# Kernel tuning notes

Hardware: AMD Instinct MI355X
Metric: run time of the kernel (lower is better)

The kernel has to match this reference:

```python
import jax, jax.numpy as jnp
import numpy as np

PERIOD = 0.1


def setup_inputs() -> dict:
    key = jax.random.key(0)
    ks = jax.random.split(key, 16)
    B, N, C, P = 2, 3072, 4, 4
    E, H, T, F, L = 512, 8, 256, 64, 4
    Nt = N // P

    def rn(k, shape, scale=0.02):
        return jax.random.normal(k, shape, jnp.float32) * scale

    return {
        "x": jax.random.normal(ks[0], (B, N, C), jnp.float32),
        "t": jax.random.normal(ks[1], (B, T), jnp.float32),
        "vec_map": jax.random.normal(ks[2], (B, N, 3), jnp.float32),
        # RelativeBias dense: freq features -> heads
        "W_rb": rn(ks[3], (F, H)),
        "b_rb": jnp.zeros((H,), jnp.float32),
        # patch embedding dense: P*C -> E
        "W_embed": rn(ks[4], (P * C, E), 0.1),
        "b_embed": jnp.zeros((E,), jnp.float32),
        "pos_emb": rn(ks[5], (Nt, E)),
        # stacked per-block params (leading dim L = n_blocks)
        "ada1_W1": rn(ks[6], (L, T, T)),
        "ada1_b1": jnp.zeros((L, T), jnp.float32),
        "ada1_W2": rn(ks[7], (L, T, 3 * E)),
        "ada1_b2": jnp.zeros((L, 3 * E), jnp.float32),
        "qkv_W": rn(ks[8], (L, E, 3 * E)),
        "qkv_b": jnp.zeros((L, 3 * E), jnp.float32),
        "out_W": rn(ks[9], (L, E, E)),
        "out_b": jnp.zeros((L, E), jnp.float32),
        "ada2_W1": rn(ks[10], (L, T, T)),
        "ada2_b1": jnp.zeros((L, T), jnp.float32),
        "ada2_W2": rn(ks[11], (L, T, 3 * E)),
        "ada2_b2": jnp.zeros((L, 3 * E), jnp.float32),
        "mlp_W1": rn(ks[12], (L, E, 4 * E)),
        "mlp_b1": jnp.zeros((L, 4 * E), jnp.float32),
        "mlp_W2": rn(ks[13], (L, 4 * E, E)),
        "mlp_b2": jnp.zeros((L, E), jnp.float32),
    }


def _layernorm(y):
    # flax LayerNorm(use_bias=False, use_scale=False), eps=1e-6
    mu = jnp.mean(y, axis=-1, keepdims=True)
    var = jnp.mean(jnp.square(y - mu), axis=-1, keepdims=True)
    return (y - mu) * jax.lax.rsqrt(var + 1e-6)


def _adaln(t, W1, b1, W2, b2):
    h = jax.nn.silu(t @ W1 + b1)
    m = (h @ W2 + b2)[..., None, :]  # (B, 1, 3E)
    return jnp.split(m, 3, axis=-1)


def reference(x, t, vec_map, W_rb, b_rb, W_embed, b_embed, pos_emb,
              ada1_W1, ada1_b1, ada1_W2, ada1_b2, qkv_W, qkv_b, out_W, out_b,
              ada2_W1, ada2_b1, ada2_W2, ada2_b2, mlp_W1, mlp_b1, mlp_W2, mlp_b2):
    B, N, C = x.shape
    Nt, E = pos_emb.shape
    P = N // Nt
    F, H = W_rb.shape
    hd = E // H

    # patchify tokens: (B, N, C) -> (B, Nt, P*C); mean vec per patch
    xp = x.reshape(B, Nt, P * C)
    vp = vec_map.reshape(B, Nt, P, 3).mean(axis=-2)

    # relative bias logits (B, Nt, Nt, H)
    v = vp / jnp.linalg.norm(vp, axis=-1, keepdims=True)
    dif = v[..., :, None, :] - v[..., None, :, :]
    dot = 1.0 - 0.5 * jnp.sum(dif * dif, axis=-1)
    angle = jnp.arccos(jnp.clip(dot, -1.0, 1.0)) / 0.005
    freqs = jnp.linspace(0, 1, F // 2) / PERIOD
    ph = freqs * angle[..., None]  # (B, Nt, Nt, F/2)
    pos = jnp.concatenate((jnp.sin(ph), jnp.cos(ph)), axis=-1)
    bias = pos @ W_rb + b_rb

    # patch embed + learned positional embedding
    h0 = xp @ W_embed + b_embed + pos_emb
    inv_sqrt_hd = 1.0 / jnp.sqrt(jnp.float32(hd))

    def block(xc, params):
        (aW1, ab1, aW2, ab2, qW, qb, oW, ob,
         cW1, cb1, cW2, cb2, mW1, mb1, mW2, mb2) = params
        g1, be1, al1 = _adaln(t, aW1, ab1, aW2, ab2)
        y = (g1 + 1.0) * _layernorm(xc) + be1
        qkv = (y @ qW + qb).reshape(B, Nt, H, 3, hd)
        q, k, vv = qkv[..., 0, :], qkv[..., 1, :], qkv[..., 2, :]
        logits = jnp.einsum('bqht,bkht->bqkh', q, k) * inv_sqrt_hd + bias
        logits = logits - jnp.max(logits, axis=-2, keepdims=True)
        attn = jax.nn.softmax(logits, axis=-2)  # softmax over keys (K axis)
        y = jnp.einsum('bqkh,bkht->bqht', attn, vv).reshape(B, Nt, E)
        y = y @ oW + ob
        xc = xc + al1 * y / jnp.sqrt(1.0 + al1 * al1)
        g2, be2, al2 = _adaln(t, cW1, cb1, cW2, cb2)
        y = (g2 + 1.0) * _layernorm(xc) + be2
        y = jax.nn.gelu(y @ mW1 + mb1) @ mW2 + mb2
        xc = xc + al2 * y / jnp.sqrt(1.0 + al2 * al2)
        return xc, None

    params = (ada1_W1, ada1_b1, ada1_W2, ada1_b2, qkv_W, qkv_b, out_W, out_b,
              ada2_W1, ada2_b1, ada2_W2, ada2_b2, mlp_W1, mlp_b1, mlp_W2, mlp_b2)
    out, _ = jax.lax.scan(block, h0, params)
    return out
```

## Files before the change

kernel.cpp:

```cpp
#include <hip/hip_runtime.h>
#include <hip/hip_bf16.h>


#define NT 768
#define EDIM 512
#define E3 1536
#define E4 2048
#define NH 8
#define TB 2

typedef unsigned short ushort_t;
typedef __attribute__((ext_vector_type(8))) short bf16x8;
typedef __attribute__((ext_vector_type(4))) float f32x4;

__device__ inline float b2f(ushort_t u) {
    unsigned int i = ((unsigned int)u) << 16; float f;
    __builtin_memcpy(&f, &i, 4); return f;
}
__device__ inline ushort_t f2b(float f) {
    __hip_bfloat16 h = __float2bfloat16(f);
    ushort_t u; __builtin_memcpy(&u, &h, 2); return u;
}
__device__ inline float gelu_tanh(float u) {
    float z = 1.5957691216057308f * (u + 0.044715f * u * u * u);
    z = fminf(z, 40.f);
    float t = __expf(z);
    float th = (t - 1.f) / (t + 1.f);
    return 0.5f * u * (1.f + th);
}

__global__ __launch_bounds__(256) void k_vnorm(const float* __restrict__ vm, float* __restrict__ v) {
    int idx = blockIdx.x * 256 + threadIdx.x;
    if (idx >= TB * NT) return;
    float s0 = 0.f, s1 = 0.f, s2 = 0.f;
    #pragma unroll
    for (int p = 0; p < 4; ++p) {
        s0 += vm[(idx * 4 + p) * 3 + 0];
        s1 += vm[(idx * 4 + p) * 3 + 1];
        s2 += vm[(idx * 4 + p) * 3 + 2];
    }
    float inv = 1.f / sqrtf(s0 * s0 + s1 * s1 + s2 * s2);
    v[idx * 3 + 0] = s0 * inv; v[idx * 3 + 1] = s1 * inv; v[idx * 3 + 2] = s2 * inv;
}

__global__ __launch_bounds__(256) void k_bias(const float* __restrict__ v, const float* __restrict__ W_rb,
                                              const float* __restrict__ b_rb, ushort_t* __restrict__ biasT) {
    int bq = blockIdx.x; int b = bq / NT, q = bq % NT;
    __shared__ float sv[NT * 3];
    int tid = threadIdx.x, lane = tid & 63, wave = tid >> 6;
    for (int i = tid; i < NT * 3; i += 256) sv[i] = v[b * NT * 3 + i];

    int g = lane >> 4, col = lane & 15;
    ushort_t tw[16];
    #pragma unroll
    for (int j = 0; j < 8; ++j) {
        float wsv = (col < 8) ? W_rb[(g * 8 + j) * 8 + col] : 0.f;
        float wcv = (col < 8) ? W_rb[(32 + g * 8 + j) * 8 + col] : 0.f;
        tw[j] = f2b(wsv); tw[8 + j] = f2b(wcv);
    }
    bf16x8 bsf, bcf;
    __builtin_memcpy(&bsf, tw, 16);
    __builtin_memcpy(&bcf, tw + 8, 16);
    float brh = (col < 8) ? b_rb[col] : 0.f;
    __syncthreads();

    float vq0 = sv[q * 3], vq1 = sv[q * 3 + 1], vq2 = sv[q * 3 + 2];
    float gf = (float)(8 * g);

    for (int it = 0; it < 12; ++it) {
        int tile = (it * 4 + wave) * 16;
        int p = tile + col;
        float d0 = vq0 - sv[p * 3], d1 = vq1 - sv[p * 3 + 1], d2 = vq2 - sv[p * 3 + 2];
        float dot = 1.f - 0.5f * (d0 * d0 + d1 * d1 + d2 * d2);
        dot = fminf(1.f, fmaxf(-1.f, dot));
        float theta = acosf(dot) * (2000.f / 31.f);
        float s1, c1; __sincosf(theta, &s1, &c1);
        float sg, cg; __sincosf(theta * gf, &sg, &cg);
        ushort_t fs[16];
        #pragma unroll
        for (int j = 0; j < 8; ++j) {
            fs[j] = f2b(sg); fs[8 + j] = f2b(cg);
            float ns = sg * c1 + cg * s1;
            cg = cg * c1 - sg * s1;
            sg = ns;
        }
        bf16x8 asf, acf;
        __builtin_memcpy(&asf, fs, 16);
        __builtin_memcpy(&acf, fs + 8, 16);
        f32x4 acc = {0.f, 0.f, 0.f, 0.f};
        acc = __builtin_amdgcn_mfma_f32_16x16x32_bf16(asf, bsf, acc, 0, 0, 0);
        acc = __builtin_amdgcn_mfma_f32_16x16x32_bf16(acf, bcf, acc, 0, 0, 0);
        if (col < 8) {
            ushort_t o[4];
            #pragma unroll
            for (int r = 0; r < 4; ++r) o[r] = f2b(acc[r] + brh);
            long off = (long)(b * 8 + col) * NT * NT + (long)q * NT + tile + 4 * g;
            uint2 pk;
            pk.x = (unsigned int)o[0] | ((unsigned int)o[1] << 16);
            pk.y = (unsigned int)o[2] | ((unsigned int)o[3] << 16);
            *(uint2*)(biasT + off) = pk;
        }
    }
}

__global__ __launch_bounds__(256) void k_embed(const float* __restrict__ x, const float* __restrict__ W,
                                               const float* __restrict__ be, const float* __restrict__ pe,
                                               float* __restrict__ xc) {
    int row = blockIdx.x; int nt = row % NT;
    __shared__ float sx[16];
    int tid = threadIdx.x;
    if (tid < 16) sx[tid] = x[row * 16 + tid];
    __syncthreads();
    for (int e = tid; e < EDIM; e += 256) {
        float a = be[e] + pe[nt * EDIM + e];
        #pragma unroll
        for (int j = 0; j < 16; ++j) a += sx[j] * W[j * EDIM + e];
        xc[(long)row * EDIM + e] = a;
    }
}

__global__ __launch_bounds__(256) void k_adaln(const float* __restrict__ t,
    const float* __restrict__ a1W1, const float* __restrict__ a1b1, const float* __restrict__ a1W2, const float* __restrict__ a1b2,
    const float* __restrict__ a2W1, const float* __restrict__ a2b1, const float* __restrict__ a2W2, const float* __restrict__ a2b2,
    float* __restrict__ ada) {
    int blk = blockIdx.x; int b = blk & 1, lw = blk >> 1; int which = lw & 1, l = lw >> 1;
    const float* W1 = (which ? a2W1 : a1W1) + (long)l * 256 * 256;
    const float* b1 = (which ? a2b1 : a1b1) + l * 256;
    const float* W2 = (which ? a2W2 : a1W2) + (long)l * 256 * E3;
    const float* b2 = (which ? a2b2 : a1b2) + l * E3;
    __shared__ float st[256], sh[256];
    int tid = threadIdx.x;
    st[tid] = t[b * 256 + tid];
    __syncthreads();
    float a = b1[tid];
    for (int i = 0; i < 256; ++i) a += st[i] * W1[i * 256 + tid];
    sh[tid] = a / (1.f + __expf(-a));
    __syncthreads();
    int c = blockIdx.y * 256 + tid;
    float m = b2[c];
    for (int i = 0; i < 256; ++i) m += sh[i] * W2[i * E3 + c];
    ada[(long)(lw * 2 + b) * E3 + c] = m;
}

__global__ __launch_bounds__(256) void k_lnmod(const float* __restrict__ xc, const float* __restrict__ ada,
                                               ushort_t* __restrict__ out, int lw) {
    int row = blockIdx.x; int b = row / NT;
    const float* ap = ada + (long)(lw * 2 + b) * E3;
    int tid = threadIdx.x;
    float2 vv = *(const float2*)(xc + (long)row * EDIM + tid * 2);
    float s1 = vv.x + vv.y, s2 = vv.x * vv.x + vv.y * vv.y;
    for (int o = 32; o; o >>= 1) { s1 += __shfl_down(s1, o); s2 += __shfl_down(s2, o); }
    __shared__ float sr[8];
    if ((tid & 63) == 0) { sr[tid >> 6] = s1; sr[4 + (tid >> 6)] = s2; }
    __syncthreads();
    s1 = sr[0] + sr[1] + sr[2] + sr[3];
    s2 = sr[4] + sr[5] + sr[6] + sr[7];
    float mu = s1 * (1.f / 512.f);
    float var = s2 * (1.f / 512.f) - mu * mu;
    float inv = rsqrtf(var + 1e-6f);
    int e = tid * 2;
    float r0 = (ap[e] + 1.f) * ((vv.x - mu) * inv) + ap[512 + e];
    float r1 = (ap[e + 1] + 1.f) * ((vv.y - mu) * inv) + ap[512 + e + 1];
    unsigned int pk = (unsigned int)f2b(r0) | ((unsigned int)f2b(r1) << 16);
    ((unsigned int*)out)[(long)row * 256 + tid] = pk;
}

__global__ __launch_bounds__(256) void k_softmax(float* __restrict__ logits) {
    float* p = logits + (long)blockIdx.x * NT;
    ushort_t* pb = (ushort_t*)p;
    int tid = threadIdx.x;
    float v0 = p[tid], v1 = p[tid + 256], v2 = p[tid + 512];
    float mx = fmaxf(v0, fmaxf(v1, v2));
    for (int o = 32; o; o >>= 1) mx = fmaxf(mx, __shfl_down(mx, o));
    __shared__ float sr[8];
    if ((tid & 63) == 0) sr[tid >> 6] = mx;
    __syncthreads();
    mx = fmaxf(fmaxf(sr[0], sr[1]), fmaxf(sr[2], sr[3]));
    float e0 = __expf(v0 - mx), e1 = __expf(v1 - mx), e2 = __expf(v2 - mx);
    float s = e0 + e1 + e2;
    for (int o = 32; o; o >>= 1) s += __shfl_down(s, o);
    if ((tid & 63) == 0) sr[4 + (tid >> 6)] = s;
    __syncthreads();
    s = sr[4] + sr[5] + sr[6] + sr[7];
    float inv = 1.f / s;
    pb[tid] = f2b(e0 * inv); pb[tid + 256] = f2b(e1 * inv); pb[tid + 512] = f2b(e2 * inv);
}

__global__ __launch_bounds__(256) void k_wT(const float* __restrict__ W, ushort_t* __restrict__ Wt,
                                            int Kd, int Nd) {
    const float* Wp = W + (long)blockIdx.z * Kd * Nd;
    ushort_t* Wtp = Wt + (long)blockIdx.z * Kd * Nd;
    int n0 = blockIdx.x * 64, k0 = blockIdx.y * 64;
    __shared__ float s[64][65];
    int tid = threadIdx.x;
    #pragma unroll
    for (int it = 0; it < 4; ++it) {
        int idx = tid + it * 256;
        int r = idx >> 4, c4 = (idx & 15) * 4;
        float4 vv = *(const float4*)(Wp + (long)(k0 + r) * Nd + n0 + c4);
        s[r][c4] = vv.x; s[r][c4 + 1] = vv.y; s[r][c4 + 2] = vv.z; s[r][c4 + 3] = vv.w;
    }
    __syncthreads();
    #pragma unroll
    for (int it = 0; it < 4; ++it) {
        int idx = tid + it * 256;
        int rn = idx >> 4, ck = (idx & 15) * 4;
        long base = (long)(n0 + rn) * Kd + k0 + ck;
        #pragma unroll
        for (int j = 0; j < 4; ++j) Wtp[base + j] = f2b(s[ck + j][rn]);
    }
}

__global__ __launch_bounds__(256) void k_vT(const ushort_t* __restrict__ qkv16, ushort_t* __restrict__ vT) {
    int bh = blockIdx.y; int b = bh >> 3, h = bh & 7;
    int nt0 = blockIdx.x * 64;
    __shared__ ushort_t s[64][80];
    int tid = threadIdx.x;
    #pragma unroll
    for (int it = 0; it < 2; ++it) {
        int idx = tid + it * 256;
        int rnt = idx >> 3, c8 = (idx & 7) * 8;
        bf16x8 vv = *(const bf16x8*)(qkv16 + ((long)(b * NT + nt0 + rnt) * E3 + h * 192 + 128 + c8));
        *(bf16x8*)&s[rnt][c8] = vv;
    }
    __syncthreads();
    #pragma unroll
    for (int it = 0; it < 2; ++it) {
        int idx = tid + it * 256;
        int d = idx >> 3, n8 = (idx & 7) * 8;
        ushort_t tmp[8];
        #pragma unroll
        for (int j = 0; j < 8; ++j) tmp[j] = s[n8 + j][d];
        bf16x8 ov; __builtin_memcpy(&ov, tmp, 16);
        *(bf16x8*)(vT + ((long)bh * 64 + d) * NT + nt0 + n8) = ov;
    }
}

__device__ inline void stC(float* C, long i, float v) { C[i] = v; }
__device__ inline void stC(ushort_t* C, long i, float v) { C[i] = f2b(v); }

template<int EPI, typename CT>
__global__ __launch_bounds__(256) void k_mm64(
        const ushort_t* __restrict__ A0, const ushort_t* __restrict__ B0,
        const void* __restrict__ biasbase, CT* __restrict__ C0,
        int Kchunk, int kSplit, int lda, int ldb, int ldc, int ldbias,
        long aB, long aH, long bB, long bH, long cB, long cH, long biB, long biH, long kcStride) {
    int z = blockIdx.z;
    int batch = z / kSplit, kc = z - batch * kSplit;
    int zb = batch >> 3, zh = batch & 7;
    const ushort_t* A = A0 + zb * aB + zh * aH + (long)kc * Kchunk;
    const ushort_t* B = B0 + zb * bB + zh * bH + (long)kc * Kchunk;
    CT* C = C0 + zb * cB + zh * cH + (EPI == 4 ? kc * kcStride : 0);

    __shared__ __align__(16) ushort_t As[64 * 64];
    __shared__ __align__(16) ushort_t Bs[64 * 64];

    int tid = threadIdx.x, lane = tid & 63, wave = tid >> 6;
    int wm = wave >> 1, wn = wave & 1;
    int m0 = blockIdx.y * 64, n0 = blockIdx.x * 64;
    int srow = lane >> 3;
    int scol = ((lane & 7) ^ srow) * 8;

    f32x4 acc[2][2];
    #pragma unroll
    for (int i = 0; i < 2; ++i)
        #pragma unroll
        for (int j = 0; j < 2; ++j) acc[i][j] = f32x4{0.f, 0.f, 0.f, 0.f};

    int r = lane & 15, g = lane >> 4, rs = r & 7;

    for (int k0 = 0; k0 < Kchunk; k0 += 64) {
        #pragma unroll
        for (int c0 = 0; c0 < 4; ++c0) {
            int c = wave * 4 + c0;
            const ushort_t* src;
            ushort_t* dst;
            if (c < 8) {
                src = A + (long)(m0 + c * 8 + srow) * lda + k0 + scol;
                dst = As + c * 512;
            } else {
                src = B + (long)(n0 + (c - 8) * 8 + srow) * ldb + k0 + scol;
                dst = Bs + (c - 8) * 512;
            }
            __builtin_amdgcn_global_load_lds(
                (const __attribute__((address_space(1))) unsigned int*)src,
                (__attribute__((address_space(3))) unsigned int*)dst, 16, 0, 0);
        }
        __syncthreads();
        bf16x8 af[2][2], bfr[2][2];
        #pragma unroll
        for (int i = 0; i < 2; ++i) {
            int row = wm * 32 + i * 16 + r;
            #pragma unroll
            for (int kh = 0; kh < 2; ++kh) {
                int sl = (kh * 4 + g) ^ rs;
                af[i][kh] = *(const bf16x8*)((const char*)As + row * 128 + sl * 16);
            }
        }
        #pragma unroll
        for (int j = 0; j < 2; ++j) {
            int row = wn * 32 + j * 16 + r;
            #pragma unroll
            for (int kh = 0; kh < 2; ++kh) {
                int sl = (kh * 4 + g) ^ rs;
                bfr[j][kh] = *(const bf16x8*)((const char*)Bs + row * 128 + sl * 16);
            }
        }
        #pragma unroll
        for (int kh = 0; kh < 2; ++kh)
            #pragma unroll
            for (int i = 0; i < 2; ++i)
                #pragma unroll
                for (int j = 0; j < 2; ++j)
                    acc[i][j] = __builtin_amdgcn_mfma_f32_16x16x32_bf16(af[i][kh], bfr[j][kh], acc[i][j], 0, 0, 0);
        __syncthreads();
    }

    int gr = (lane >> 4) * 4, cL = lane & 15;
    #pragma unroll
    for (int i = 0; i < 2; ++i) {
        int mB = m0 + wm * 32 + i * 16 + gr;
        #pragma unroll
        for (int j = 0; j < 2; ++j) {
            int n = n0 + wn * 32 + j * 16 + cL;
            float bn = 0.f;
            if constexpr (EPI == 0 || EPI == 1) {
                if (biasbase) bn = ((const float*)biasbase)[n];
            }
            #pragma unroll
            for (int rr = 0; rr < 4; ++rr) {
                float vv = acc[i][j][rr];
                long cidx = (long)(mB + rr) * ldc + n;
                if constexpr (EPI == 0) {
                    stC(C, cidx, vv + bn);
                } else if constexpr (EPI == 1) {
                    stC(C, cidx, gelu_tanh(vv + bn));
                } else if constexpr (EPI == 2) {
                    const ushort_t* bp = (const ushort_t*)biasbase + zb * biB + zh * biH;
                    stC(C, cidx, vv * 0.125f + b2f(bp[(long)(mB + rr) * ldbias + n]));
                } else {
                    stC(C, cidx, vv);
                }
            }
        }
    }
}

__global__ __launch_bounds__(256) void k_red_res(const float* __restrict__ P, int kSplit,
        const float* __restrict__ bias, const float* __restrict__ ada, int lw,
        const float* __restrict__ xin, float* __restrict__ xout) {
    int gidx = blockIdx.x * 256 + threadIdx.x;
    int e4 = gidx * 4;
    int m = e4 >> 9, n = e4 & 511;
    int b = (m >= NT);
    const float* al = ada + (long)(lw * 2 + b) * E3 + 1024;
    float4 s = *(const float4*)(P + e4);
    for (int kc = 1; kc < kSplit; ++kc) {
        float4 p = *(const float4*)(P + (long)kc * 786432 + e4);
        s.x += p.x; s.y += p.y; s.z += p.z; s.w += p.w;
    }
    float4 bv = *(const float4*)(bias + n);
    float4 av = *(const float4*)(al + n);
    float4 xv = *(const float4*)(xin + e4);
    float4 r;
    r.x = xv.x + av.x * rsqrtf(1.f + av.x * av.x) * (s.x + bv.x);
    r.y = xv.y + av.y * rsqrtf(1.f + av.y * av.y) * (s.y + bv.y);
    r.z = xv.z + av.z * rsqrtf(1.f + av.z * av.z) * (s.z + bv.z);
    r.w = xv.w + av.w * rsqrtf(1.f + av.w * av.w) * (s.w + bv.w);
    *(float4*)(xout + e4) = r;
}

__global__ __launch_bounds__(256) void k_red_pv(const float* __restrict__ P, ushort_t* __restrict__ attnb) {
    int blk = blockIdx.x;
    int bh = blk / 48, sub = blk % 48;
    int inner = sub * 256 + threadIdx.x;
    int nt = inner >> 4, d = (inner & 15) * 4;
    long src = (long)bh * 49152 + nt * 64 + d;
    float4 s = *(const float4*)(P + src);
    #pragma unroll
    for (int kc = 1; kc < 4; ++kc) {
        float4 p = *(const float4*)(P + (long)kc * 786432 + src);
        s.x += p.x; s.y += p.y; s.z += p.z; s.w += p.w;
    }
    int b = bh >> 3, h = bh & 7;
    long off = ((long)(b * NT + nt) * EDIM) + h * 64 + d;
    unsigned int p0 = (unsigned int)f2b(s.x) | ((unsigned int)f2b(s.y) << 16);
    unsigned int p1 = (unsigned int)f2b(s.z) | ((unsigned int)f2b(s.w) << 16);
    unsigned int* dst = (unsigned int*)(attnb + off);
    dst[0] = p0; dst[1] = p1;
}

extern "C" void kernel_launch(void* const* d_in, const int* in_sizes, int n_in,
                              void* d_out, int out_size, void* d_ws, size_t ws_size,
                              hipStream_t stream) {
    const float* x       = (const float*)d_in[0];
    const float* t       = (const float*)d_in[1];
    const float* vec_map = (const float*)d_in[2];
    const float* W_rb    = (const float*)d_in[3];
    const float* b_rb    = (const float*)d_in[4];
    const float* W_embed = (const float*)d_in[5];
    const float* b_embed = (const float*)d_in[6];
    const float* pos_emb = (const float*)d_in[7];
    const float* a1W1    = (const float*)d_in[8];
    const float* a1b1    = (const float*)d_in[9];
    const float* a1W2    = (const float*)d_in[10];
    const float* a1b2    = (const float*)d_in[11];
    const float* qkv_W   = (const float*)d_in[12];
    const float* qkv_b   = (const float*)d_in[13];
    const float* out_W   = (const float*)d_in[14];
    const float* out_b   = (const float*)d_in[15];
    const float* a2W1    = (const float*)d_in[16];
    const float* a2b1    = (const float*)d_in[17];
    const float* a2W2    = (const float*)d_in[18];
    const float* a2b2    = (const float*)d_in[19];
    const float* mlp_W1  = (const float*)d_in[20];
    const float* mlp_b1  = (const float*)d_in[21];
    const float* mlp_W2  = (const float*)d_in[22];
    const float* mlp_b2  = (const float*)d_in[23];

    float* ws = (float*)d_ws;
    size_t o = 0;
    float* v        = ws + o; o += 8192;
    ushort_t* biasT = (ushort_t*)(ws + o); o += 4718592;
    float* logits   = ws + o; o += 9437184;
    float* ada      = ws + o; o += 24576;
    float* xc       = ws + o; o += 786432;
    ushort_t* ln16  = (ushort_t*)(ws + o); o += 393216;
    ushort_t* qkv16 = (ushort_t*)(ws + o); o += 1179648;
    ushort_t* vT    = (ushort_t*)(ws + o); o += 393216;
    ushort_t* attnb = (ushort_t*)(ws + o); o += 393216;
    ushort_t* mlph  = (ushort_t*)(ws + o); o += 1572864;
    ushort_t* qkvWt = (ushort_t*)(ws + o); o += 1572864;
    ushort_t* outWt = (ushort_t*)(ws + o); o += 524288;
    ushort_t* mlp1Wt = (ushort_t*)(ws + o); o += 2097152;
    ushort_t* mlp2Wt = (ushort_t*)(ws + o); o += 2097152;
    float* P_pv     = ws + o; o += 3145728;
    float* P_proj   = ws + o; o += 3145728;

    k_vnorm<<<6, 256, 0, stream>>>(vec_map, v);
    k_bias<<<TB * NT, 256, 0, stream>>>(v, W_rb, b_rb, biasT);
    k_embed<<<TB * NT, 256, 0, stream>>>(x, W_embed, b_embed, pos_emb, xc);
    k_adaln<<<dim3(16, 6), 256, 0, stream>>>(t, a1W1, a1b1, a1W2, a1b2, a2W1, a2b1, a2W2, a2b2, ada);
    k_wT<<<dim3(24, 8, 4), 256, 0, stream>>>(qkv_W,  qkvWt,  512, 1536);
    k_wT<<<dim3(8,  8, 4), 256, 0, stream>>>(out_W,  outWt,  512, 512);
    k_wT<<<dim3(32, 8, 4), 256, 0, stream>>>(mlp_W1, mlp1Wt, 512, 2048);
    k_wT<<<dim3(8, 32, 4), 256, 0, stream>>>(mlp_W2, mlp2Wt, 2048, 512);

    const long qB = (long)NT * E3, qH = 192;
    const long lB = (long)NH * NT * NT, lH = (long)NT * NT;
    const long pB = 2 * lB, pH = 2 * lH;
    const long vB = (long)NH * 64 * NT, vH = (long)64 * NT;

    for (int l = 0; l < 4; ++l) {
        int lw0 = l * 2, lw1 = l * 2 + 1;
        k_lnmod<<<TB * NT, 256, 0, stream>>>(xc, ada, ln16, lw0);
        k_mm64<0, ushort_t><<<dim3(24, 24, 1), 256, 0, stream>>>(
            ln16, qkvWt + (long)l * 786432, qkv_b + l * E3, qkv16,
            512, 1, 512, 512, E3, 0, 0, 0, 0, 0, 0, 0, 0, 0, 0);
        k_vT<<<dim3(12, 16), 256, 0, stream>>>(qkv16, vT);
        k_mm64<2, float><<<dim3(12, 12, 16), 256, 0, stream>>>(
            qkv16, qkv16 + 64, biasT, logits,
            64, 1, E3, E3, NT, NT, qB, qH, qB, qH, lB, lH, lB, lH, 0);
        k_softmax<<<TB * NH * NT, 256, 0, stream>>>(logits);
        k_mm64<4, float><<<dim3(1, 12, 64), 256, 0, stream>>>(
            (const ushort_t*)logits, vT, nullptr, P_pv,
            192, 4, E3, NT, 64, 0, pB, pH, vB, vH, (long)NH * 49152, 49152, 0, 0, 786432);
        k_red_pv<<<768, 256, 0, stream>>>(P_pv, attnb);
        k_mm64<4, float><<<dim3(8, 24, 2), 256, 0, stream>>>(
            attnb, outWt + (long)l * 262144, nullptr, P_proj,
            256, 2, 512, 512, EDIM, 0, 0, 0, 0, 0, 0, 0, 0, 0, 786432);
        k_red_res<<<768, 256, 0, stream>>>(P_proj, 2, out_b + l * EDIM, ada, lw0, xc, xc);
        k_lnmod<<<TB * NT, 256, 0, stream>>>(xc, ada, ln16, lw1);
        k_mm64<1, ushort_t><<<dim3(32, 24, 1), 256, 0, stream>>>(
            ln16, mlp1Wt + (long)l * 1048576, mlp_b1 + l * E4, mlph,
            512, 1, 512, 512, E4, 0, 0, 0, 0, 0, 0, 0, 0, 0, 0);
        k_mm64<4, float><<<dim3(8, 24, 4), 256, 0, stream>>>(
            mlph, mlp2Wt + (long)l * 1048576, nullptr, P_proj,
            512, 4, 2048, 2048, EDIM, 0, 0, 0, 0, 0, 0, 0, 0, 0, 786432);
        k_red_res<<<768, 256, 0, stream>>>(P_proj, 4, mlp_b2 + l * EDIM, ada, lw1, xc,
            (l == 3) ? (float*)d_out : xc);
    }
}
```

Measured before the change: 431.1 us.

## Fuse attention into flash-style kernel and switch GEMMs to 128x128 tiles with fused residual epilogue

```diff
diff --git a/kernel.cpp b/kernel.cpp
--- a/kernel.cpp
+++ b/kernel.cpp
@@ -12,6 +12,10 @@
 typedef unsigned short ushort_t;
 typedef __attribute__((ext_vector_type(8))) short bf16x8;
 typedef __attribute__((ext_vector_type(4))) float f32x4;
+
+#define GLOAD(src, dst) __builtin_amdgcn_global_load_lds( \
+    (const __attribute__((address_space(1))) unsigned int*)(src), \
+    (__attribute__((address_space(3))) unsigned int*)(dst), 16, 0, 0)
 
 __device__ inline float b2f(ushort_t u) {
     unsigned int i = ((unsigned int)u) << 16; float f;
@@ -165,27 +169,6 @@
     ((unsigned int*)out)[(long)row * 256 + tid] = pk;
 }
 
-__global__ __launch_bounds__(256) void k_softmax(float* __restrict__ logits) {
-    float* p = logits + (long)blockIdx.x * NT;
-    ushort_t* pb = (ushort_t*)p;
-    int tid = threadIdx.x;
-    float v0 = p[tid], v1 = p[tid + 256], v2 = p[tid + 512];
-    float mx = fmaxf(v0, fmaxf(v1, v2));
-    for (int o = 32; o; o >>= 1) mx = fmaxf(mx, __shfl_down(mx, o));
-    __shared__ float sr[8];
-    if ((tid & 63) == 0) sr[tid >> 6] = mx;
-    __syncthreads();
-    mx = fmaxf(fmaxf(sr[0], sr[1]), fmaxf(sr[2], sr[3]));
-    float e0 = __expf(v0 - mx), e1 = __expf(v1 - mx), e2 = __expf(v2 - mx);
-    float s = e0 + e1 + e2;
-    for (int o = 32; o; o >>= 1) s += __shfl_down(s, o);
-    if ((tid & 63) == 0) sr[4 + (tid >> 6)] = s;
-    __syncthreads();
-    s = sr[4] + sr[5] + sr[6] + sr[7];
-    float inv = 1.f / s;
-    pb[tid] = f2b(e0 * inv); pb[tid + 256] = f2b(e1 * inv); pb[tid + 512] = f2b(e2 * inv);
-}
-
 __global__ __launch_bounds__(256) void k_wT(const float* __restrict__ W, ushort_t* __restrict__ Wt,
                                             int Kd, int Nd) {
     const float* Wp = W + (long)blockIdx.z * Kd * Nd;
@@ -236,158 +219,226 @@
     }
 }
 
-__device__ inline void stC(float* C, long i, float v) { C[i] = v; }
-__device__ inline void stC(ushort_t* C, long i, float v) { C[i] = f2b(v); }
-
-template<int EPI, typename CT>
-__global__ __launch_bounds__(256) void k_mm64(
+__global__ __launch_bounds__(256) void k_attn(const ushort_t* __restrict__ qkv16,
+        const ushort_t* __restrict__ vT, const ushort_t* __restrict__ biasT,
+        ushort_t* __restrict__ attnb) {
+    int qt = blockIdx.x, bh = blockIdx.y;
+    int b = bh >> 3, h = bh & 7;
+    __shared__ __align__(16) ushort_t Ks[4096];
+    __shared__ __align__(16) ushort_t Vs[4096];
+    __shared__ __align__(16) ushort_t Bi[4096];
+    int tid = threadIdx.x, lane = tid & 63, wave = tid >> 6;
+    int g = lane >> 4, c = lane & 15;
+    int ls = lane & 7, lr = lane >> 3;
+    int stg_col = (ls ^ lr) * 8;
+    int q0 = qt * 64;
+
+    bf16x8 aq[2];
+    {
+        const ushort_t* qp = qkv16 + ((long)(b * NT + q0 + wave * 16 + c) * E3) + h * 192;
+        aq[0] = *(const bf16x8*)(qp + g * 8);
+        aq[1] = *(const bf16x8*)(qp + 32 + g * 8);
+    }
+    float m_r[4], l_r[4];
+    f32x4 o_acc[4];
+    #pragma unroll
+    for (int rr = 0; rr < 4; ++rr) { m_r[rr] = -1e30f; l_r[rr] = 0.f; }
+    #pragma unroll
+    for (int nf = 0; nf < 4; ++nf) o_acc[nf] = f32x4{0.f, 0.f, 0.f, 0.f};
+
+    for (int kt = 0; kt < 12; ++kt) {
+        int k0 = kt * 64;
+        #pragma unroll
+        for (int is = 0; is < 2; ++is) {
+            int row = is * 32 + wave * 8 + lr;
+            int dstb = (is * 32 + wave * 8) * 64;
+            GLOAD(qkv16 + (long)(b * NT + k0 + row) * E3 + h * 192 + 64 + stg_col, Ks + dstb);
+            GLOAD(vT + ((long)bh * 64 + row) * NT + k0 + stg_col, Vs + dstb);
+            GLOAD(biasT + (long)bh * NT * NT + (long)(q0 + row) * NT + k0 + ls * 8, Bi + dstb);
+        }
+        __syncthreads();
+        f32x4 s[4];
+        #pragma unroll
+        for (int nf = 0; nf < 4; ++nf) {
+            s[nf] = f32x4{0.f, 0.f, 0.f, 0.f};
+            #pragma unroll
+            for (int kh = 0; kh < 2; ++kh) {
+                int row = nf * 16 + c;
+                bf16x8 bk = *(const bf16x8*)(Ks + row * 64 + (((kh * 4 + g) ^ (row & 7))) * 8);
+                s[nf] = __builtin_amdgcn_mfma_f32_16x16x32_bf16(aq[kh], bk, s[nf], 0, 0, 0);
+            }
+        }
+        float p[4][4], mt[4];
+        #pragma unroll
+        for (int rr = 0; rr < 4; ++rr) {
+            int ql = wave * 16 + g * 4 + rr;
+            #pragma unroll
+            for (int nf = 0; nf < 4; ++nf)
+                p[nf][rr] = s[nf][rr] * 0.125f + b2f(Bi[ql * 64 + nf * 16 + c]);
+            float mx = fmaxf(fmaxf(p[0][rr], p[1][rr]), fmaxf(p[2][rr], p[3][rr]));
+            mx = fmaxf(mx, __shfl_xor(mx, 1));
+            mx = fmaxf(mx, __shfl_xor(mx, 2));
+            mx = fmaxf(mx, __shfl_xor(mx, 4));
+            mx = fmaxf(mx, __shfl_xor(mx, 8));
+            mt[rr] = mx;
+        }
+        #pragma unroll
+        for (int rr = 0; rr < 4; ++rr) {
+            float mnew = fmaxf(m_r[rr], mt[rr]);
+            float sc = __expf(m_r[rr] - mnew);
+            m_r[rr] = mnew;
+            float rsum = 0.f;
+            #pragma unroll
+            for (int nf = 0; nf < 4; ++nf) {
+                p[nf][rr] = __expf(p[nf][rr] - mnew);
+                rsum += p[nf][rr];
+            }
+            rsum += __shfl_xor(rsum, 1); rsum += __shfl_xor(rsum, 2);
+            rsum += __shfl_xor(rsum, 4); rsum += __shfl_xor(rsum, 8);
+            l_r[rr] = l_r[rr] * sc + rsum;
+            #pragma unroll
+            for (int nf = 0; nf < 4; ++nf) o_acc[nf][rr] *= sc;
+        }
+        #pragma unroll
+        for (int nf = 0; nf < 4; ++nf) {
+            int kl = nf * 16 + c;
+            int slot = kl >> 3, win = kl & 7;
+            #pragma unroll
+            for (int rr = 0; rr < 4; ++rr) {
+                int ql = wave * 16 + g * 4 + rr;
+                Bi[ql * 64 + ((slot ^ (ql & 7)) * 8) + win] = f2b(p[nf][rr]);
+            }
+        }
+        asm volatile("s_waitcnt lgkmcnt(0)" ::: "memory");
+        bf16x8 ap[2];
+        #pragma unroll
+        for (int kh = 0; kh < 2; ++kh) {
+            int ql = wave * 16 + c;
+            ap[kh] = *(const bf16x8*)(Bi + ql * 64 + (((kh * 4 + g) ^ (ql & 7))) * 8);
+        }
+        #pragma unroll
+        for (int nf = 0; nf < 4; ++nf) {
+            #pragma unroll
+            for (int kh = 0; kh < 2; ++kh) {
+                int row = nf * 16 + c;
+                bf16x8 bv = *(const bf16x8*)(Vs + row * 64 + (((kh * 4 + g) ^ (row & 7))) * 8);
+                o_acc[nf] = __builtin_amdgcn_mfma_f32_16x16x32_bf16(ap[kh], bv, o_acc[nf], 0, 0, 0);
+            }
+        }
+        __syncthreads();
+    }
+    #pragma unroll
+    for (int nf = 0; nf < 4; ++nf) {
+        #pragma unroll
+        for (int rr = 0; rr < 4; ++rr) {
+            int ql = wave * 16 + g * 4 + rr;
+            Ks[ql * 64 + nf * 16 + c] = f2b(o_acc[nf][rr] / l_r[rr]);
+        }
+    }
+    asm volatile("s_waitcnt lgkmcnt(0)" ::: "memory");
+    __syncthreads();
+    int orow = wave * 16 + (lane >> 2);
+    int ocol = (lane & 3) * 16;
+    const ushort_t* srcO = Ks + orow * 64 + ocol;
+    ushort_t* dstO = attnb + (long)(b * NT + q0 + orow) * EDIM + h * 64 + ocol;
+    *(bf16x8*)(dstO) = *(const bf16x8*)(srcO);
+    *(bf16x8*)(dstO + 8) = *(const bf16x8*)(srcO + 8);
+}
+
+template<int EPI>
+__global__ __launch_bounds__(256) void k_mm128(
         const ushort_t* __restrict__ A0, const ushort_t* __restrict__ B0,
-        const void* __restrict__ biasbase, CT* __restrict__ C0,
-        int Kchunk, int kSplit, int lda, int ldb, int ldc, int ldbias,
-        long aB, long aH, long bB, long bH, long cB, long cH, long biB, long biH, long kcStride) {
-    int z = blockIdx.z;
-    int batch = z / kSplit, kc = z - batch * kSplit;
-    int zb = batch >> 3, zh = batch & 7;
-    const ushort_t* A = A0 + zb * aB + zh * aH + (long)kc * Kchunk;
-    const ushort_t* B = B0 + zb * bB + zh * bH + (long)kc * Kchunk;
-    CT* C = C0 + zb * cB + zh * cH + (EPI == 4 ? kc * kcStride : 0);
-
-    __shared__ __align__(16) ushort_t As[64 * 64];
-    __shared__ __align__(16) ushort_t Bs[64 * 64];
-
+        const float* __restrict__ bias, const float* __restrict__ xin,
+        const float* __restrict__ ada, int lw,
+        void* __restrict__ C0,
+        int K, int lda, int ldb, int ldc) {
+    __shared__ __align__(16) ushort_t As[128 * 64];
+    __shared__ __align__(16) ushort_t Bs[128 * 64];
     int tid = threadIdx.x, lane = tid & 63, wave = tid >> 6;
     int wm = wave >> 1, wn = wave & 1;
-    int m0 = blockIdx.y * 64, n0 = blockIdx.x * 64;
-    int srow = lane >> 3;
-    int scol = ((lane & 7) ^ srow) * 8;
-
-    f32x4 acc[2][2];
-    #pragma unroll
-    for (int i = 0; i < 2; ++i)
-        #pragma unroll
-        for (int j = 0; j < 2; ++j) acc[i][j] = f32x4{0.f, 0.f, 0.f, 0.f};
-
+    int m0 = blockIdx.y * 128, n0 = blockIdx.x * 128;
+    int ls = lane & 7, lr = lane >> 3;
+    int stg_col = (ls ^ lr) * 8;
     int r = lane & 15, g = lane >> 4, rs = r & 7;
 
-    for (int k0 = 0; k0 < Kchunk; k0 += 64) {
+    f32x4 acc[4][4];
+    #pragma unroll
+    for (int i = 0; i < 4; ++i)
+        #pragma unroll
+        for (int j = 0; j < 4; ++j) acc[i][j] = f32x4{0.f, 0.f, 0.f, 0.f};
+
+    for (int k0 = 0; k0 < K; k0 += 64) {
         #pragma unroll
         for (int c0 = 0; c0 < 4; ++c0) {
-            int c = wave * 4 + c0;
-            const ushort_t* src;
-            ushort_t* dst;
-            if (c < 8) {
-                src = A + (long)(m0 + c * 8 + srow) * lda + k0 + scol;
-                dst = As + c * 512;
-            } else {
-                src = B + (long)(n0 + (c - 8) * 8 + srow) * ldb + k0 + scol;
-                dst = Bs + (c - 8) * 512;
-            }
-            __builtin_amdgcn_global_load_lds(
-                (const __attribute__((address_space(1))) unsigned int*)src,
-                (__attribute__((address_space(3))) unsigned int*)dst, 16, 0, 0);
+            int ch = wave * 4 + c0;
+            GLOAD(A0 + (long)(m0 + ch * 8 + lr) * lda + k0 + stg_col, As + ch * 512);
+            GLOAD(B0 + (long)(n0 + ch * 8 + lr) * ldb + k0 + stg_col, Bs + ch * 512);
         }
         __syncthreads();
-        bf16x8 af[2][2], bfr[2][2];
-        #pragma unroll
-        for (int i = 0; i < 2; ++i) {
-            int row = wm * 32 + i * 16 + r;
-            #pragma unroll
-            for (int kh = 0; kh < 2; ++kh) {
-                int sl = (kh * 4 + g) ^ rs;
-                af[i][kh] = *(const bf16x8*)((const char*)As + row * 128 + sl * 16);
-            }
-        }
-        #pragma unroll
-        for (int j = 0; j < 2; ++j) {
-            int row = wn * 32 + j * 16 + r;
-            #pragma unroll
-            for (int kh = 0; kh < 2; ++kh) {
-                int sl = (kh * 4 + g) ^ rs;
-                bfr[j][kh] = *(const bf16x8*)((const char*)Bs + row * 128 + sl * 16);
-            }
+        bf16x8 af[4][2], bf[4][2];
+        #pragma unroll
+        for (int i = 0; i < 4; ++i) {
+            int row = wm * 64 + i * 16 + r;
+            #pragma unroll
+            for (int kh = 0; kh < 2; ++kh)
+                af[i][kh] = *(const bf16x8*)(As + row * 64 + (((kh * 4 + g) ^ rs)) * 8);
+        }
+        #pragma unroll
+        for (int j = 0; j < 4; ++j) {
+            int row = wn * 64 + j * 16 + r;
+            #pragma unroll
+            for (int kh = 0; kh < 2; ++kh)
+                bf[j][kh] = *(const bf16x8*)(Bs + row * 64 + (((kh * 4 + g) ^ rs)) * 8);
         }
         #pragma unroll
         for (int kh = 0; kh < 2; ++kh)
             #pragma unroll
-            for (int i = 0; i < 2; ++i)
+            for (int i = 0; i < 4; ++i)
                 #pragma unroll
-                for (int j = 0; j < 2; ++j)
-                    acc[i][j] = __builtin_amdgcn_mfma_f32_16x16x32_bf16(af[i][kh], bfr[j][kh], acc[i][j], 0, 0, 0);
+                for (int j = 0; j < 4; ++j)
+                    acc[i][j] = __builtin_amdgcn_mfma_f32_16x16x32_bf16(af[i][kh], bf[j][kh], acc[i][j], 0, 0, 0);
         __syncthreads();
     }
 
-    int gr = (lane >> 4) * 4, cL = lane & 15;
-    #pragma unroll
-    for (int i = 0; i < 2; ++i) {
-        int mB = m0 + wm * 32 + i * 16 + gr;
-        #pragma unroll
-        for (int j = 0; j < 2; ++j) {
-            int n = n0 + wn * 32 + j * 16 + cL;
-            float bn = 0.f;
-            if constexpr (EPI == 0 || EPI == 1) {
-                if (biasbase) bn = ((const float*)biasbase)[n];
-            }
-            #pragma unroll
-            for (int rr = 0; rr < 4; ++rr) {
-                float vv = acc[i][j][rr];
-                long cidx = (long)(mB + rr) * ldc + n;
-                if constexpr (EPI == 0) {
-                    stC(C, cidx, vv + bn);
-                } else if constexpr (EPI == 1) {
-                    stC(C, cidx, gelu_tanh(vv + bn));
-                } else if constexpr (EPI == 2) {
-                    const ushort_t* bp = (const ushort_t*)biasbase + zb * biB + zh * biH;
-                    stC(C, cidx, vv * 0.125f + b2f(bp[(long)(mB + rr) * ldbias + n]));
-                } else {
-                    stC(C, cidx, vv);
+    int gr4 = g * 4, cL = lane & 15;
+    if constexpr (EPI == 0 || EPI == 1) {
+        ushort_t* C = (ushort_t*)C0;
+        #pragma unroll
+        for (int i = 0; i < 4; ++i) {
+            int mrow = m0 + wm * 64 + i * 16 + gr4;
+            #pragma unroll
+            for (int j = 0; j < 4; ++j) {
+                int n = n0 + wn * 64 + j * 16 + cL;
+                float bn = bias[n];
+                #pragma unroll
+                for (int rr = 0; rr < 4; ++rr) {
+                    float vv = acc[i][j][rr] + bn;
+                    if constexpr (EPI == 1) vv = gelu_tanh(vv);
+                    C[(long)(mrow + rr) * ldc + n] = f2b(vv);
                 }
             }
         }
-    }
-}
-
-__global__ __launch_bounds__(256) void k_red_res(const float* __restrict__ P, int kSplit,
-        const float* __restrict__ bias, const float* __restrict__ ada, int lw,
-        const float* __restrict__ xin, float* __restrict__ xout) {
-    int gidx = blockIdx.x * 256 + threadIdx.x;
-    int e4 = gidx * 4;
-    int m = e4 >> 9, n = e4 & 511;
-    int b = (m >= NT);
-    const float* al = ada + (long)(lw * 2 + b) * E3 + 1024;
-    float4 s = *(const float4*)(P + e4);
-    for (int kc = 1; kc < kSplit; ++kc) {
-        float4 p = *(const float4*)(P + (long)kc * 786432 + e4);
-        s.x += p.x; s.y += p.y; s.z += p.z; s.w += p.w;
-    }
-    float4 bv = *(const float4*)(bias + n);
-    float4 av = *(const float4*)(al + n);
-    float4 xv = *(const float4*)(xin + e4);
-    float4 r;
-    r.x = xv.x + av.x * rsqrtf(1.f + av.x * av.x) * (s.x + bv.x);
-    r.y = xv.y + av.y * rsqrtf(1.f + av.y * av.y) * (s.y + bv.y);
-    r.z = xv.z + av.z * rsqrtf(1.f + av.z * av.z) * (s.z + bv.z);
-    r.w = xv.w + av.w * rsqrtf(1.f + av.w * av.w) * (s.w + bv.w);
-    *(float4*)(xout + e4) = r;
-}
-
-__global__ __launch_bounds__(256) void k_red_pv(const float* __restrict__ P, ushort_t* __restrict__ attnb) {
-    int blk = blockIdx.x;
-    int bh = blk / 48, sub = blk % 48;
-    int inner = sub * 256 + threadIdx.x;
-    int nt = inner >> 4, d = (inner & 15) * 4;
-    long src = (long)bh * 49152 + nt * 64 + d;
-    float4 s = *(const float4*)(P + src);
-    #pragma unroll
-    for (int kc = 1; kc < 4; ++kc) {
-        float4 p = *(const float4*)(P + (long)kc * 786432 + src);
-        s.x += p.x; s.y += p.y; s.z += p.z; s.w += p.w;
-    }
-    int b = bh >> 3, h = bh & 7;
-    long off = ((long)(b * NT + nt) * EDIM) + h * 64 + d;
-    unsigned int p0 = (unsigned int)f2b(s.x) | ((unsigned int)f2b(s.y) << 16);
-    unsigned int p1 = (unsigned int)f2b(s.z) | ((unsigned int)f2b(s.w) << 16);
-    unsigned int* dst = (unsigned int*)(attnb + off);
-    dst[0] = p0; dst[1] = p1;
+    } else {
+        float* C = (float*)C0;
+        #pragma unroll
+        for (int i = 0; i < 4; ++i) {
+            int mrow = m0 + wm * 64 + i * 16 + gr4;
+            int bb = (mrow >= NT) ? 1 : 0;
+            const float* al = ada + (long)(lw * 2 + bb) * E3 + 1024;
+            #pragma unroll
+            for (int j = 0; j < 4; ++j) {
+                int n = n0 + wn * 64 + j * 16 + cL;
+                float a = al[n];
+                float sc = a * rsqrtf(1.f + a * a);
+                float bn = bias[n];
+                #pragma unroll
+                for (int rr = 0; rr < 4; ++rr) {
+                    long idx = (long)(mrow + rr) * ldc + n;
+                    C[idx] = xin[idx] + sc * (acc[i][j][rr] + bn);
+                }
+            }
+        }
+    }
 }
 
 extern "C" void kernel_launch(void* const* d_in, const int* in_sizes, int n_in,
@@ -422,7 +473,6 @@
     size_t o = 0;
     float* v        = ws + o; o += 8192;
     ushort_t* biasT = (ushort_t*)(ws + o); o += 4718592;
-    float* logits   = ws + o; o += 9437184;
     float* ada      = ws + o; o += 24576;
     float* xc       = ws + o; o += 786432;
     ushort_t* ln16  = (ushort_t*)(ws + o); o += 393216;
@@ -434,8 +484,6 @@
     ushort_t* outWt = (ushort_t*)(ws + o); o += 524288;
     ushort_t* mlp1Wt = (ushort_t*)(ws + o); o += 2097152;
     ushort_t* mlp2Wt = (ushort_t*)(ws + o); o += 2097152;
-    float* P_pv     = ws + o; o += 3145728;
-    float* P_proj   = ws + o; o += 3145728;
 
     k_vnorm<<<6, 256, 0, stream>>>(vec_map, v);
     k_bias<<<TB * NT, 256, 0, stream>>>(v, W_rb, b_rb, biasT);
@@ -446,38 +494,23 @@
     k_wT<<<dim3(32, 8, 4), 256, 0, stream>>>(mlp_W1, mlp1Wt, 512, 2048);
     k_wT<<<dim3(8, 32, 4), 256, 0, stream>>>(mlp_W2, mlp2Wt, 2048, 512);
 
-    const long qB = (long)NT * E3, qH = 192;
-    const long lB = (long)NH * NT * NT, lH = (long)NT * NT;
-    const long pB = 2 * lB, pH = 2 * lH;
-    const long vB = (long)NH * 64 * NT, vH = (long)64 * NT;
-
     for (int l = 0; l < 4; ++l) {
         int lw0 = l * 2, lw1 = l * 2 + 1;
         k_lnmod<<<TB * NT, 256, 0, stream>>>(xc, ada, ln16, lw0);
-        k_mm64<0, ushort_t><<<dim3(24, 24, 1), 256, 0, stream>>>(
-            ln16, qkvWt + (long)l * 786432, qkv_b + l * E3, qkv16,
-            512, 1, 512, 512, E3, 0, 0, 0, 0, 0, 0, 0, 0, 0, 0);
+        k_mm128<0><<<dim3(12, 12), 256, 0, stream>>>(
+            ln16, qkvWt + (long)l * 786432, qkv_b + l * E3, nullptr, nullptr, 0,
+            qkv16, 512, 512, 512, E3);
         k_vT<<<dim3(12, 16), 256, 0, stream>>>(qkv16, vT);
-        k_mm64<2, float><<<dim3(12, 12, 16), 256, 0, stream>>>(
-            qkv16, qkv16 + 64, biasT, logits,
-            64, 1, E3, E3, NT, NT, qB, qH, qB, qH, lB, lH, lB, lH, 0);
-        k_softmax<<<TB * NH * NT, 256, 0, stream>>>(logits);
-        k_mm64<4, float><<<dim3(1, 12, 64), 256, 0, stream>>>(
-            (const ushort_t*)logits, vT, nullptr, P_pv,
-            192, 4, E3, NT, 64, 0, pB, pH, vB, vH, (long)NH * 49152, 49152, 0, 0, 786432);
-        k_red_pv<<<768, 256, 0, stream>>>(P_pv, attnb);
-        k_mm64<4, float><<<dim3(8, 24, 2), 256, 0, stream>>>(
-            attnb, outWt + (long)l * 262144, nullptr, P_proj,
-            256, 2, 512, 512, EDIM, 0, 0, 0, 0, 0, 0, 0, 0, 0, 786432);
-        k_red_res<<<768, 256, 0, stream>>>(P_proj, 2, out_b + l * EDIM, ada, lw0, xc, xc);
+        k_attn<<<dim3(12, 16), 256, 0, stream>>>(qkv16, vT, biasT, attnb);
+        k_mm128<5><<<dim3(4, 12), 256, 0, stream>>>(
+            attnb, outWt + (long)l * 262144, out_b + l * EDIM, xc, ada, lw0,
+            xc, 512, 512, 512, EDIM);
         k_lnmod<<<TB * NT, 256, 0, stream>>>(xc, ada, ln16, lw1);
-        k_mm64<1, ushort_t><<<dim3(32, 24, 1), 256, 0, stream>>>(
-            ln16, mlp1Wt + (long)l * 1048576, mlp_b1 + l * E4, mlph,
-            512, 1, 512, 512, E4, 0, 0, 0, 0, 0, 0, 0, 0, 0, 0);
-        k_mm64<4, float><<<dim3(8, 24, 4), 256, 0, stream>>>(
-            mlph, mlp2Wt + (long)l * 1048576, nullptr, P_proj,
-            512, 4, 2048, 2048, EDIM, 0, 0, 0, 0, 0, 0, 0, 0, 0, 786432);
-        k_red_res<<<768, 256, 0, stream>>>(P_proj, 4, mlp_b2 + l * EDIM, ada, lw1, xc,
-            (l == 3) ? (float*)d_out : xc);
-    }
-}
+        k_mm128<1><<<dim3(16, 12), 256, 0, stream>>>(
+            ln16, mlp1Wt + (long)l * 1048576, mlp_b1 + l * E4, nullptr, nullptr, 0,
+            mlph, 512, 512, 512, E4);
+        k_mm128<5><<<dim3(4, 12), 256, 0, stream>>>(
+            mlph, mlp2Wt + (long)l * 1048576, mlp_b2 + l * EDIM, xc, ada, lw1,
+            (l == 3) ? (float*)d_out : xc, 2048, 2048, 2048, EDIM);
+    }
+}
```

Measured after the change: 522.0 us. 21.1% more time.
